# Kernel optimization log

Measured on AMD Instinct MI355X. Metric: run time of the kernel, lower is better.

Reference implementation:

```python
import jax, jax.numpy as jnp
import numpy as np
import math

B, S, D = 16, 256, 1024   # batch, seq (= s_model), d_model
HP, HC = 16, 8
DK, SK = D // HP, S // HC
EPS = 1e-6


def setup_inputs() -> dict:
    key = jax.random.key(0)
    ks = jax.random.split(key, 3)
    x = jax.random.normal(ks[0], (B, S, D), dtype=jnp.float32)
    Wp = jax.random.normal(ks[1], (3, D, D), dtype=jnp.float32) * 0.02  # (in,out)
    bp = jnp.zeros((3, D), dtype=jnp.float32)
    Wc = jax.random.normal(ks[2], (4, S, S), dtype=jnp.float32) * 0.02  # (in,out)
    bc = jnp.zeros((4, S), dtype=jnp.float32)
    a_p = jnp.ones((D,), dtype=jnp.float32)
    b_p = jnp.zeros((D,), dtype=jnp.float32)
    a_c = jnp.ones((S,), dtype=jnp.float32)
    b_c = jnp.zeros((S,), dtype=jnp.float32)
    return {"x": x, "Wp": Wp, "bp": bp, "Wc": Wc, "bc": bc,
            "a_p": a_p, "b_p": b_p, "a_c": a_c, "b_c": b_c}


def _std(x, axis):
    # torch .std(): unbiased (ddof=1)
    return jnp.std(x, axis=axis, keepdims=True, ddof=1)


def _attn(q, k, v):
    # q,k,v: [B, H, T, dk]; dropout is identity (eval)
    scores = jnp.einsum('bhtd,bhsd->bhts', q, k) / math.sqrt(q.shape[-1])
    p = jax.nn.softmax(scores, axis=-1)
    return jnp.einsum('bhts,bhsd->bhtd', p, v)


def reference(x, Wp, bp, Wc, bc, a_p, b_p, a_c, b_c):
    nb = x.shape[0]
    # ---- LayerNorm over channels (norm_p) ----
    mean = jnp.mean(x, axis=-1, keepdims=True)
    xp = a_p * (x - mean) / (_std(x, -1) + EPS) + b_p            # [B,S,D]
    # ---- positional attention over sequence ----
    qkv = jnp.einsum('bsd,nde->nbse', xp, Wp) + bp[:, None, None, :]
    q, k, v = [t.reshape(nb, S, HP, DK).transpose(0, 2, 1, 3) for t in qkv]
    xp = _attn(q, k, v).transpose(0, 2, 1, 3).reshape(nb, S, D)  # [B,S,D]
    # ---- LayerNorm_C: stats over sequence dim, affine indexed by seq ----
    mean_c = jnp.mean(xp, axis=-2, keepdims=True)                # [B,1,D]
    xc = a_c[:, None] * (xp - mean_c) / (_std(xp, -2) + EPS) + b_c[:, None]
    # ---- channel attention: channels are tokens, head dim SK ----
    xt = xc.transpose(0, 2, 1)                                    # [B,D,S]
    qkvc = jnp.einsum('bds,nse->nbde', xt, Wc[:3]) + bc[:3, None, None, :]
    qc, kc, vc = [t.reshape(nb, D, HC, SK).transpose(0, 2, 1, 3) for t in qkvc]
    xcatt = _attn(qc, kc, vc).transpose(0, 2, 1, 3).reshape(nb, D, S)  # [B,D,S]
    out = jnp.einsum('bds,se->bde', xcatt, Wc[3]) + bc[3]         # [B,D,S]
    return out.transpose(0, 2, 1)                                  # [B,S,D]
```

## Files before the change

### kernel.cpp

```cpp
#include <hip/hip_runtime.h>
#include <hip/hip_bf16.h>
#include <math.h>

#define B_ 16
#define S_ 256
#define D_ 1024
#define HP_ 16
#define DK_ 64
#define HC_ 8
#define SK_ 32
#define EPS_ 1e-6f

typedef __attribute__((ext_vector_type(8))) short short8v;
typedef __attribute__((ext_vector_type(4))) float f32x4;

__device__ __forceinline__ unsigned short f2bf(float f) {
    unsigned u = __float_as_uint(f);
    u += 0x7fffu + ((u >> 16) & 1u);
    return (unsigned short)(u >> 16);
}
__device__ __forceinline__ float bf2f(unsigned short h) {
    return __uint_as_float((unsigned)h << 16);
}
__device__ __forceinline__ ushort2 f2bf2(float a, float b) {
    __hip_bfloat162 h = __float22bfloat162_rn(make_float2(a, b));
    union { __hip_bfloat162 h2; ushort2 u2; } cv;
    cv.h2 = h;
    return cv.u2;
}
__device__ __forceinline__ void ldlds16(const unsigned short* g, unsigned short* l) {
    const unsigned int* gp = reinterpret_cast<const unsigned int*>(g);
    auto* lp = reinterpret_cast<__attribute__((address_space(3))) unsigned int*>(
        reinterpret_cast<uintptr_t>(l));
    __builtin_amdgcn_global_load_lds(gp, lp, 16, 0, 0);
}

__global__ __launch_bounds__(256) void k1_ln_p(
    const float* __restrict__ x, const float* __restrict__ a_p,
    const float* __restrict__ b_p, unsigned short* __restrict__ xh,
    unsigned short* __restrict__ xl)
{
    const int row = blockIdx.x;
    const float4* xr = (const float4*)(x + (size_t)row * D_);
    const int tid = threadIdx.x;
    float4 v = xr[tid];
    float s  = v.x + v.y + v.z + v.w;
    float sq = v.x*v.x + v.y*v.y + v.z*v.z + v.w*v.w;
    #pragma unroll
    for (int off = 32; off > 0; off >>= 1) {
        s  += __shfl_down(s, off);
        sq += __shfl_down(sq, off);
    }
    __shared__ float red[8];
    const int wid = tid >> 6, lane = tid & 63;
    if (lane == 0) { red[wid] = s; red[4 + wid] = sq; }
    __syncthreads();
    if (tid == 0) {
        float S0 = red[0] + red[1] + red[2] + red[3];
        float Q0 = red[4] + red[5] + red[6] + red[7];
        float mean = S0 / (float)D_;
        float var  = fmaxf((Q0 - (float)D_ * mean * mean) / (float)(D_ - 1), 0.0f);
        red[0] = mean;
        red[1] = 1.0f / (sqrtf(var) + EPS_);
    }
    __syncthreads();
    const float mean = red[0], inv = red[1];
    float4 a = ((const float4*)a_p)[tid];
    float4 b = ((const float4*)b_p)[tid];
    float o0 = a.x * (v.x - mean) * inv + b.x;
    float o1 = a.y * (v.y - mean) * inv + b.y;
    float o2 = a.z * (v.z - mean) * inv + b.z;
    float o3 = a.w * (v.w - mean) * inv + b.w;
    ushort2 h01 = f2bf2(o0, o1), h23 = f2bf2(o2, o3);
    ushort2 l01 = f2bf2(o0 - bf2f(h01.x), o1 - bf2f(h01.y));
    ushort2 l23 = f2bf2(o2 - bf2f(h23.x), o3 - bf2f(h23.y));
    ushort4 hv, lv;
    hv.x = h01.x; hv.y = h01.y; hv.z = h23.x; hv.w = h23.y;
    lv.x = l01.x; lv.y = l01.y; lv.z = l23.x; lv.w = l23.y;
    *(ushort4*)&xh[(size_t)row * D_ + tid*4] = hv;
    *(ushort4*)&xl[(size_t)row * D_ + tid*4] = lv;
}

__global__ __launch_bounds__(256) void tsplit(
    const float* __restrict__ W, unsigned short* __restrict__ Th,
    unsigned short* __restrict__ Tl, int K, int N)
{
    const int z = blockIdx.z;
    W  += (size_t)z * K * N;
    Th += (size_t)z * K * N;
    Tl += (size_t)z * K * N;
    const int k0 = blockIdx.x * 64, n0 = blockIdx.y * 64;
    __shared__ float tile[64][65];
    const int ix = threadIdx.x & 63, iy = threadIdx.x >> 6;
    #pragma unroll
    for (int u = 0; u < 16; u++) {
        const int kk = iy*16 + u;
        tile[kk][ix] = W[(size_t)(k0+kk)*N + n0 + ix];
    }
    __syncthreads();
    #pragma unroll
    for (int u = 0; u < 16; u += 2) {
        const int nn0 = iy*16 + u, nn1 = nn0 + 1;
        const float v0 = tile[ix][nn0], v1 = tile[ix][nn1];
        ushort2 h2 = f2bf2(v0, v1);
        ushort2 l2 = f2bf2(v0 - bf2f(h2.x), v1 - bf2f(h2.y));
        Th[(size_t)(n0+nn0)*K + k0 + ix] = h2.x;
        Th[(size_t)(n0+nn1)*K + k0 + ix] = h2.y;
        Tl[(size_t)(n0+nn0)*K + k0 + ix] = l2.x;
        Tl[(size_t)(n0+nn1)*K + k0 + ix] = l2.y;
    }
}

template<int OUTMODE>
__global__ __launch_bounds__(256) void mm_mfma(
    const unsigned short* __restrict__ Ah, const unsigned short* __restrict__ Al,
    const unsigned short* __restrict__ Bh, const unsigned short* __restrict__ Bl,
    const float* __restrict__ bias, void* __restrict__ Cout,
    int M, int N, int K, long sB, long sBias, long sC, long loff, int TB)
{
    const int z = blockIdx.z;
    Bh   += (size_t)z * sB;
    Bl   += (size_t)z * sB;
    bias += (size_t)z * sBias;
    const int n0 = blockIdx.x * 128, m0 = blockIdx.y * 128;
    __shared__ __align__(16) unsigned short Ash[128*32], Als[128*32];
    __shared__ __align__(16) unsigned short Bsh[128*32], Bls[128*32];
    const int tid = threadIdx.x;
    const int wave = tid >> 6, lane = tid & 63;
    const int wm = wave & 1, wn = wave >> 1;
    const int lrow = lane & 15, quad = lane >> 4;
    size_t gaOff[2], gbOff[2];
    int cb[2];
    #pragma unroll
    for (int j = 0; j < 2; j++) {
        const int p = wave*128 + j*64 + lane;
        const int row = p >> 2;
        const int cc = (p & 3) ^ ((row >> 1) & 3);
        gaOff[j] = (size_t)(m0 + row) * K + cc*8;
        gbOff[j] = (size_t)(n0 + row) * K + cc*8;
        cb[j] = (wave*128 + j*64) * 8;
    }
    int aFr[4], bFr[4];
    #pragma unroll
    for (int i = 0; i < 4; i++) {
        const int ra = wm*64 + i*16 + lrow;
        aFr[i] = ((ra << 2) | (quad ^ ((ra >> 1) & 3))) * 8;
        const int rb = wn*64 + i*16 + lrow;
        bFr[i] = ((rb << 2) | (quad ^ ((rb >> 1) & 3))) * 8;
    }
    f32x4 acc[4][4];
    #pragma unroll
    for (int j = 0; j < 4; j++) {
        const float bv = bias[n0 + wn*64 + j*16 + lrow];
        #pragma unroll
        for (int i = 0; i < 4; i++) {
            acc[i][j][0] = bv; acc[i][j][1] = bv; acc[i][j][2] = bv; acc[i][j][3] = bv;
        }
    }
    for (int k0 = 0; k0 < K; k0 += 32) {
        __syncthreads();
        #pragma unroll
        for (int j = 0; j < 2; j++) {
            ldlds16(Ah + gaOff[j] + k0, &Ash[cb[j]]);
            ldlds16(Al + gaOff[j] + k0, &Als[cb[j]]);
            ldlds16(Bh + gbOff[j] + k0, &Bsh[cb[j]]);
            ldlds16(Bl + gbOff[j] + k0, &Bls[cb[j]]);
        }
        __syncthreads();
        short8v bhf[4], blf[4];
        #pragma unroll
        for (int j = 0; j < 4; j++) {
            bhf[j] = *(const short8v*)&Bsh[bFr[j]];
            blf[j] = *(const short8v*)&Bls[bFr[j]];
        }
        #pragma unroll
        for (int i = 0; i < 4; i++) {
            short8v ahf = *(const short8v*)&Ash[aFr[i]];
            short8v alf = *(const short8v*)&Als[aFr[i]];
            #pragma unroll
            for (int j = 0; j < 4; j++) {
                acc[i][j] = __builtin_amdgcn_mfma_f32_16x16x32_bf16(ahf, bhf[j], acc[i][j], 0, 0, 0);
                acc[i][j] = __builtin_amdgcn_mfma_f32_16x16x32_bf16(ahf, blf[j], acc[i][j], 0, 0, 0);
                acc[i][j] = __builtin_amdgcn_mfma_f32_16x16x32_bf16(alf, bhf[j], acc[i][j], 0, 0, 0);
            }
        }
    }
    #pragma unroll
    for (int i = 0; i < 4; i++) {
        const int mrow = m0 + wm*64 + i*16 + quad*4;
        #pragma unroll
        for (int j = 0; j < 4; j++) {
            const int ncol = n0 + wn*64 + j*16 + lrow;
            if (OUTMODE == 0) {
                float* C = (float*)Cout + (size_t)z * sC;
                #pragma unroll
                for (int r = 0; r < 4; r++)
                    C[(size_t)(mrow + r) * N + ncol] = acc[i][j][r];
            } else if (OUTMODE == 1) {
                unsigned short* Ch = (unsigned short*)Cout + (size_t)z * sC;
                unsigned short* Cl = Ch + loff;
                #pragma unroll
                for (int r = 0; r < 4; r += 2) {
                    const float v0 = acc[i][j][r], v1 = acc[i][j][r+1];
                    ushort2 h2 = f2bf2(v0, v1);
                    ushort2 l2 = f2bf2(v0 - bf2f(h2.x), v1 - bf2f(h2.y));
                    Ch[(size_t)(mrow + r    ) * N + ncol] = h2.x;
                    Ch[(size_t)(mrow + r + 1) * N + ncol] = h2.y;
                    Cl[(size_t)(mrow + r    ) * N + ncol] = l2.x;
                    Cl[(size_t)(mrow + r + 1) * N + ncol] = l2.y;
                }
            } else if (OUTMODE == 2) {
                unsigned short* Ch = (unsigned short*)Cout;
                unsigned short* Cl = Ch + loff;
                const int bidx = mrow / TB, t0 = mrow % TB;
                const size_t ad = (size_t)bidx * N * TB + (size_t)ncol * TB + t0;
                const float v0 = acc[i][j][0], v1 = acc[i][j][1];
                const float v2 = acc[i][j][2], v3 = acc[i][j][3];
                ushort2 h01 = f2bf2(v0, v1), h23 = f2bf2(v2, v3);
                ushort2 l01 = f2bf2(v0 - bf2f(h01.x), v1 - bf2f(h01.y));
                ushort2 l23 = f2bf2(v2 - bf2f(h23.x), v3 - bf2f(h23.y));
                ushort4 hv, lv;
                hv.x = h01.x; hv.y = h01.y; hv.z = h23.x; hv.w = h23.y;
                lv.x = l01.x; lv.y = l01.y; lv.z = l23.x; lv.w = l23.y;
                *(ushort4*)&Ch[ad] = hv;
                *(ushort4*)&Cl[ad] = lv;
            } else {
                float* C = (float*)Cout;
                const int bidx = mrow / TB, t0 = mrow % TB;
                f32x4 a4 = acc[i][j];
                *(float4*)&C[((size_t)bidx * N + ncol) * TB + t0] = *(float4*)&a4;
            }
        }
    }
}

__global__ __launch_bounds__(256) void k3_mfma(
    const unsigned short* __restrict__ qh, const unsigned short* __restrict__ ql,
    const unsigned short* __restrict__ kh, const unsigned short* __restrict__ kl,
    const unsigned short* __restrict__ vth, const unsigned short* __restrict__ vtl,
    float* __restrict__ out)
{
    const int m0 = blockIdx.x * 64;
    const int h = blockIdx.y, b = blockIdx.z;
    const int hoff = h * DK_;
    const size_t rowb = (size_t)b * S_;
    __shared__ __align__(16) unsigned short Ksh[64*64], Ksl[64*64];
    __shared__ __align__(16) unsigned short VTh[64*64], VTl[64*64];
    __shared__ __align__(16) unsigned short Ps[64][72];
    const int tid = threadIdx.x;
    const int w = tid >> 6, lane = tid & 63;
    const int lrow = lane & 15, quad = lane >> 4;
    short8v bqh[2], bql[2];
    #pragma unroll
    for (int ks = 0; ks < 2; ks++) {
        const size_t qb = (rowb + m0 + w*16 + lrow) * D_ + hoff + ks*32 + quad*8;
        bqh[ks] = *(const short8v*)&qh[qb];
        bql[ks] = *(const short8v*)&ql[qb];
    }
    size_t kOff[2], vOff[2];
    int cb[2];
    #pragma unroll
    for (int j = 0; j < 2; j++) {
        const int p = w*128 + j*64 + lane;
        const int row = p >> 3;
        const int cc = (p & 7) ^ (row & 7);
        kOff[j] = (rowb + row) * D_ + hoff + cc*8;
        vOff[j] = ((size_t)b * D_ + hoff + row) * S_ + cc*8;
        cb[j] = (w*128 + j*64) * 8;
    }
    f32x4 o[4] = {};
    float lacc = 0.f;
    for (int kt = 0; kt < 4; kt++) {
        const int n00 = kt * 64;
        __syncthreads();
        #pragma unroll
        for (int j = 0; j < 2; j++) {
            ldlds16(kh  + kOff[j] + (size_t)n00 * D_, &Ksh[cb[j]]);
            ldlds16(kl  + kOff[j] + (size_t)n00 * D_, &Ksl[cb[j]]);
            ldlds16(vth + vOff[j] + n00,              &VTh[cb[j]]);
            ldlds16(vtl + vOff[j] + n00,              &VTl[cb[j]]);
        }
        __syncthreads();
        f32x4 sa[4] = {};
        #pragma unroll
        for (int ks = 0; ks < 2; ks++) {
            #pragma unroll
            for (int jk = 0; jk < 4; jk++) {
                const int r = jk*16 + lrow, c = ks*4 + quad;
                const int off = ((r << 3) | (c ^ (r & 7))) * 8;
                short8v akh = *(const short8v*)&Ksh[off];
                short8v akl = *(const short8v*)&Ksl[off];
                sa[jk] = __builtin_amdgcn_mfma_f32_16x16x32_bf16(akh, bqh[ks], sa[jk], 0, 0, 0);
                sa[jk] = __builtin_amdgcn_mfma_f32_16x16x32_bf16(akl, bqh[ks], sa[jk], 0, 0, 0);
                sa[jk] = __builtin_amdgcn_mfma_f32_16x16x32_bf16(akh, bql[ks], sa[jk], 0, 0, 0);
            }
        }
        #pragma unroll
        for (int jk = 0; jk < 4; jk++) {
            float p0 = __expf(sa[jk][0] * 0.125f);
            float p1 = __expf(sa[jk][1] * 0.125f);
            float p2 = __expf(sa[jk][2] * 0.125f);
            float p3 = __expf(sa[jk][3] * 0.125f);
            lacc += (p0 + p1) + (p2 + p3);
            ushort2 p01 = f2bf2(p0, p1), p23 = f2bf2(p2, p3);
            ushort4 ph;
            ph.x = p01.x; ph.y = p01.y; ph.z = p23.x; ph.w = p23.y;
            *(ushort4*)&Ps[w*16 + lrow][jk*16 + quad*4] = ph;
        }
        #pragma unroll
        for (int ks = 0; ks < 2; ks++) {
            short8v ap = *(const short8v*)&Ps[w*16 + lrow][ks*32 + quad*8];
            #pragma unroll
            for (int nf = 0; nf < 4; nf++) {
                const int r = nf*16 + lrow, c = ks*4 + quad;
                const int off = ((r << 3) | (c ^ (r & 7))) * 8;
                short8v vH = *(const short8v*)&VTh[off];
                short8v vL = *(const short8v*)&VTl[off];
                o[nf] = __builtin_amdgcn_mfma_f32_16x16x32_bf16(ap, vH, o[nf], 0, 0, 0);
                o[nf] = __builtin_amdgcn_mfma_f32_16x16x32_bf16(ap, vL, o[nf], 0, 0, 0);
            }
        }
    }
    lacc += __shfl_xor(lacc, 16);
    lacc += __shfl_xor(lacc, 32);
    #pragma unroll
    for (int r = 0; r < 4; r++) {
        const float linv = 1.0f / __shfl(lacc, quad*4 + r);
        #pragma unroll
        for (int nf = 0; nf < 4; nf++)
            out[(rowb + m0 + w*16 + quad*4 + r) * D_ + hoff + nf*16 + lrow] =
                o[nf][r] * linv;
    }
}

__global__ __launch_bounds__(256) void k6_mfma(
    const unsigned short* __restrict__ qch, const unsigned short* __restrict__ qcl,
    const unsigned short* __restrict__ kch, const unsigned short* __restrict__ kcl,
    const unsigned short* __restrict__ vth, const unsigned short* __restrict__ vtl,
    unsigned short* __restrict__ oh, unsigned short* __restrict__ ol)
{
    const int m0 = blockIdx.x * 128;
    const int h = blockIdx.y, b = blockIdx.z;
    const int hoff = h * SK_;
    const size_t rowb = (size_t)b * D_;
    __shared__ __align__(16) unsigned short Ksh[64*32], Ksl[64*32];
    __shared__ __align__(16) unsigned short VTh[32*64], VTl[32*64];
    __shared__ __align__(16) unsigned short Ps[128][72];
    const int tid = threadIdx.x;
    const int w = tid >> 6, lane = tid & 63;
    const int lrow = lane & 15, quad = lane >> 4;
    short8v bqh[2], bql[2];
    #pragma unroll
    for (int i = 0; i < 2; i++) {
        const size_t qb = (rowb + m0 + w*32 + i*16 + lrow) * S_ + hoff + quad*8;
        bqh[i] = *(const short8v*)&qch[qb];
        bql[i] = *(const short8v*)&qcl[qb];
    }
    size_t kOff, vOff;
    {
        const int pK = w*64 + lane;
        const int rowK = pK >> 2;
        const int ccK = (pK & 3) ^ ((rowK >> 1) & 3);
        kOff = (rowb + rowK) * S_ + hoff + ccK*8;
        const int pV = w*64 + lane;
        const int rowV = pV >> 3;
        const int ccV = (pV & 7) ^ (rowV & 7);
        vOff = ((size_t)b * S_ + hoff + rowV) * D_ + ccV*8;
    }
    const int cb = w*64*8;
    f32x4 o[2][2] = {};
    float lacc[2] = {0.f, 0.f};
    for (int kt = 0; kt < 16; kt++) {
        const int n00 = kt * 64;
        __syncthreads();
        ldlds16(kch + kOff + (size_t)n00 * S_, &Ksh[cb]);
        ldlds16(kcl + kOff + (size_t)n00 * S_, &Ksl[cb]);
        ldlds16(vth + vOff + n00,              &VTh[cb]);
        ldlds16(vtl + vOff + n00,              &VTl[cb]);
        __syncthreads();
        f32x4 sa[2][4] = {};
        #pragma unroll
        for (int jk = 0; jk < 4; jk++) {
            const int r = jk*16 + lrow;
            const int off = ((r << 2) | (quad ^ ((r >> 1) & 3))) * 8;
            short8v akh = *(const short8v*)&Ksh[off];
            short8v akl = *(const short8v*)&Ksl[off];
            #pragma unroll
            for (int i = 0; i < 2; i++) {
                sa[i][jk] = __builtin_amdgcn_mfma_f32_16x16x32_bf16(akh, bqh[i], sa[i][jk], 0, 0, 0);
                sa[i][jk] = __builtin_amdgcn_mfma_f32_16x16x32_bf16(akl, bqh[i], sa[i][jk], 0, 0, 0);
                sa[i][jk] = __builtin_amdgcn_mfma_f32_16x16x32_bf16(akh, bql[i], sa[i][jk], 0, 0, 0);
            }
        }
        #pragma unroll
        for (int i = 0; i < 2; i++)
            #pragma unroll
            for (int jk = 0; jk < 4; jk++) {
                float p0 = __expf(sa[i][jk][0] * 0.17677669529663687f);
                float p1 = __expf(sa[i][jk][1] * 0.17677669529663687f);
                float p2 = __expf(sa[i][jk][2] * 0.17677669529663687f);
                float p3 = __expf(sa[i][jk][3] * 0.17677669529663687f);
                lacc[i] += (p0 + p1) + (p2 + p3);
                ushort2 p01 = f2bf2(p0, p1), p23 = f2bf2(p2, p3);
                ushort4 ph;
                ph.x = p01.x; ph.y = p01.y; ph.z = p23.x; ph.w = p23.y;
                *(ushort4*)&Ps[w*32 + i*16 + lrow][jk*16 + quad*4] = ph;
            }
        #pragma unroll
        for (int ks = 0; ks < 2; ks++) {
            short8v ap[2];
            #pragma unroll
            for (int i = 0; i < 2; i++)
                ap[i] = *(const short8v*)&Ps[w*32 + i*16 + lrow][ks*32 + quad*8];
            #pragma unroll
            for (int nf = 0; nf < 2; nf++) {
                const int r = nf*16 + lrow, c = ks*4 + quad;
                const int off = ((r << 3) | (c ^ (r & 7))) * 8;
                short8v vHf = *(const short8v*)&VTh[off];
                short8v vLf = *(const short8v*)&VTl[off];
                #pragma unroll
                for (int i = 0; i < 2; i++) {
                    o[i][nf] = __builtin_amdgcn_mfma_f32_16x16x32_bf16(ap[i], vHf, o[i][nf], 0, 0, 0);
                    o[i][nf] = __builtin_amdgcn_mfma_f32_16x16x32_bf16(ap[i], vLf, o[i][nf], 0, 0, 0);
                }
            }
        }
    }
    #pragma unroll
    for (int i = 0; i < 2; i++) {
        lacc[i] += __shfl_xor(lacc[i], 16);
        lacc[i] += __shfl_xor(lacc[i], 32);
    }
    #pragma unroll
    for (int i = 0; i < 2; i++)
        #pragma unroll
        for (int r = 0; r < 4; r++) {
            const float linv = 1.0f / __shfl(lacc[i], quad*4 + r);
            const float v0 = o[i][0][r] * linv;
            const float v1 = o[i][1][r] * linv;
            ushort2 h2 = f2bf2(v0, v1);
            ushort2 l2 = f2bf2(v0 - bf2f(h2.x), v1 - bf2f(h2.y));
            const size_t idx =
                (rowb + m0 + w*32 + i*16 + quad*4 + r) * S_ + hoff + lrow;
            oh[idx]      = h2.x;
            oh[idx + 16] = h2.y;
            ol[idx]      = l2.x;
            ol[idx + 16] = l2.y;
        }
}

__global__ __launch_bounds__(256) void k4_fused(
    const float* __restrict__ x, const float* __restrict__ a_c,
    const float* __restrict__ b_c, unsigned short* __restrict__ xth,
    unsigned short* __restrict__ xtl)
{
    const int d0 = blockIdx.x * 64, b = blockIdx.y;
    __shared__ float tile[256][65];
    __shared__ float part[8][64];
    __shared__ float stats[2][64];
    __shared__ float acs[256], bcs[256];
    const int tid = threadIdx.x;
    acs[tid] = a_c[tid];
    bcs[tid] = b_c[tid];
    const int dl = tid & 63, sq = tid >> 6;
    float s1 = 0.f, s2 = 0.f;
    #pragma unroll 8
    for (int u = 0; u < 64; u++) {
        const int srow = sq*64 + u;
        const float v = x[((size_t)(b*S_ + srow))*D_ + d0 + dl];
        tile[srow][dl] = v;
        s1 += v; s2 += v*v;
    }
    part[sq][dl] = s1; part[4+sq][dl] = s2;
    __syncthreads();
    if (tid < 64) {
        const float S = part[0][tid]+part[1][tid]+part[2][tid]+part[3][tid];
        const float Q = part[4][tid]+part[5][tid]+part[6][tid]+part[7][tid];
        const float mean = S / (float)S_;
        const float var  = fmaxf((Q - (float)S_*mean*mean)/(float)(S_-1), 0.f);
        stats[0][tid] = mean;
        stats[1][tid] = 1.f/(sqrtf(var)+EPS_);
    }
    __syncthreads();
    const int dd = tid >> 2, s00 = (tid & 3) * 64;
    const float mean = stats[0][dd], inv = stats[1][dd];
    const size_t obase = ((size_t)(b*D_ + d0 + dd))*S_ + s00;
    #pragma unroll
    for (int c = 0; c < 8; c++) {
        union { ushort u[8]; uint4 v4; } hb, lb;
        #pragma unroll
        for (int t = 0; t < 8; t += 2) {
            const int s = s00 + c*8 + t;
            const float v0 = acs[s]  *(tile[s][dd]  -mean)*inv + bcs[s];
            const float v1 = acs[s+1]*(tile[s+1][dd]-mean)*inv + bcs[s+1];
            ushort2 h2 = f2bf2(v0, v1);
            ushort2 l2 = f2bf2(v0 - bf2f(h2.x), v1 - bf2f(h2.y));
            hb.u[t] = h2.x; hb.u[t+1] = h2.y;
            lb.u[t] = l2.x; lb.u[t+1] = l2.y;
        }
        *(uint4*)&xth[obase + c*8] = hb.v4;
        *(uint4*)&xtl[obase + c*8] = lb.v4;
    }
}

extern "C" void kernel_launch(void* const* d_in, const int* in_sizes, int n_in,
                              void* d_out, int out_size, void* d_ws, size_t ws_size,
                              hipStream_t stream)
{
    const float* x   = (const float*)d_in[0];
    const float* Wp  = (const float*)d_in[1];
    const float* bp  = (const float*)d_in[2];
    const float* Wc  = (const float*)d_in[3];
    const float* bc  = (const float*)d_in[4];
    const float* a_p = (const float*)d_in[5];
    const float* b_p = (const float*)d_in[6];
    const float* a_c = (const float*)d_in[7];
    const float* b_c = (const float*)d_in[8];
    float* out = (float*)d_out;
    float* ws  = (float*)d_ws;
    const size_t NE = (size_t)B_ * S_ * D_;

    float* S0 = ws;
    float* S1 = ws + NE;
    float* S2 = ws + 2*NE;
    float* S3 = ws + 3*NE;
    unsigned short* SW = (unsigned short*)(ws + 4*NE);

    const size_t baseBytes = 4*NE*sizeof(float);
    const bool big = ws_size >= baseBytes + (size_t)2 * 3 * D_ * D_ * sizeof(unsigned short) * 2;

    unsigned short* xh = (unsigned short*)S0;
    unsigned short* xl = xh + NE;
    unsigned short* q_h  = (unsigned short*)S1;
    unsigned short* k_h  = (unsigned short*)S2;
    unsigned short* vt_h = (unsigned short*)S3;

    k1_ln_p<<<dim3(B_*S_), 256, 0, stream>>>(x, a_p, b_p, xh, xl);

    if (big) {
        unsigned short* WTh = SW;
        unsigned short* WTl = WTh + (size_t)3 * D_ * D_;
        tsplit<<<dim3(D_/64, D_/64, 3), 256, 0, stream>>>(Wp, WTh, WTl, D_, D_);
        mm_mfma<1><<<dim3(D_/128, (B_*S_)/128, 2), 256, 0, stream>>>(
            xh, xl, WTh, WTl, bp, (void*)q_h,
            B_*S_, D_, D_, (long)D_*D_, (long)D_, (long)(2*NE), (long)NE, 1);
        mm_mfma<2><<<dim3(D_/128, (B_*S_)/128, 1), 256, 0, stream>>>(
            xh, xl, WTh + (size_t)2*D_*D_, WTl + (size_t)2*D_*D_, bp + 2*D_,
            (void*)vt_h, B_*S_, D_, D_, 0, 0, 0, (long)NE, S_);
    } else {
        unsigned short* WTh = SW;
        unsigned short* WTl = WTh + (size_t)D_ * D_;
        for (int z = 0; z < 3; z++) {
            tsplit<<<dim3(D_/64, D_/64, 1), 256, 0, stream>>>(
                Wp + (size_t)z*D_*D_, WTh, WTl, D_, D_);
            if (z < 2)
                mm_mfma<1><<<dim3(D_/128, (B_*S_)/128, 1), 256, 0, stream>>>(
                    xh, xl, WTh, WTl, bp + (size_t)z*D_,
                    (void*)(q_h + (size_t)z*2*NE),
                    B_*S_, D_, D_, 0, 0, 0, (long)NE, 1);
            else
                mm_mfma<2><<<dim3(D_/128, (B_*S_)/128, 1), 256, 0, stream>>>(
                    xh, xl, WTh, WTl, bp + (size_t)z*D_, (void*)vt_h,
                    B_*S_, D_, D_, 0, 0, 0, (long)NE, S_);
        }
    }

    k3_mfma<<<dim3(S_/64, HP_, B_), 256, 0, stream>>>(
        q_h, q_h + NE, k_h, k_h + NE, vt_h, vt_h + NE, S0);

    unsigned short* xth = (unsigned short*)S1;
    k4_fused<<<dim3(D_/64, B_), 256, 0, stream>>>(S0, a_c, b_c, xth, xth + NE);

    unsigned short* WcTh = SW;
    unsigned short* WcTl = WcTh + (size_t)4 * S_ * S_;
    tsplit<<<dim3(S_/64, S_/64, 4), 256, 0, stream>>>(Wc, WcTh, WcTl, S_, S_);
    unsigned short* qc_h  = (unsigned short*)S2;
    unsigned short* vct_h = (unsigned short*)S0;
    mm_mfma<1><<<dim3(S_/128, (B_*D_)/128, 2), 256, 0, stream>>>(
        xth, xth + NE, WcTh, WcTl, bc, (void*)qc_h,
        B_*D_, S_, S_, (long)S_*S_, (long)S_, (long)(2*NE), (long)NE, 1);
    mm_mfma<2><<<dim3(S_/128, (B_*D_)/128, 1), 256, 0, stream>>>(
        xth, xth + NE, WcTh + (size_t)2*S_*S_, WcTl + (size_t)2*S_*S_, bc + 2*S_,
        (void*)vct_h, B_*D_, S_, S_, 0, 0, 0, (long)NE, D_);

    unsigned short* kc_h = (unsigned short*)S3;
    unsigned short* xch  = (unsigned short*)S1;
    k6_mfma<<<dim3(D_/128, HC_, B_), 256, 0, stream>>>(
        qc_h, qc_h + NE, kc_h, kc_h + NE, vct_h, vct_h + NE, xch, xch + NE);

    mm_mfma<3><<<dim3(S_/128, (B_*D_)/128, 1), 256, 0, stream>>>(
        xch, xch + NE, WcTh + (size_t)3*S_*S_, WcTl + (size_t)3*S_*S_, bc + 3*S_,
        (void*)out, B_*D_, S_, S_, 0, 0, 0, 0, D_);
}
```

Baseline: 356.5 us.

## Double-buffer attention K/V tiles, fold softmax scale into QK projections, swizzle blocks

Both attention kernels now use two LDS buffers for K/V, so the next tile's global-to-LDS load is issued before computing on the current one. The two full barriers per iteration become a single waitcnt plus barrier. The softmax scale times log2(e) is split as a square root into the Q and K projection epilogues, which lets the kernels call a raw v_exp_f32 instead of __expf with a multiply. The block index mapping is also remapped so that consecutive workgroups are spread across batch/head. The costs are doubled LDS use, which may reduce occupancy, and slightly different rounding of Q and K.

```diff
diff --git a/kernel.cpp b/kernel.cpp
--- a/kernel.cpp
+++ b/kernel.cpp
@@ -11,6 +11,9 @@
 #define SK_ 32
 #define EPS_ 1e-6f
 
+#define ALPHA_P 0.42466089973135876f
+#define ALPHA_C 0.50500991942f
+
 typedef __attribute__((ext_vector_type(8))) short short8v;
 typedef __attribute__((ext_vector_type(4))) float f32x4;
 
@@ -27,6 +30,11 @@
     union { __hip_bfloat162 h2; ushort2 u2; } cv;
     cv.h2 = h;
     return cv.u2;
+}
+__device__ __forceinline__ float exp2_fast(float x) {
+    float r;
+    asm("v_exp_f32 %0, %1\n\ts_nop 0" : "=v"(r) : "v"(x));
+    return r;
 }
 __device__ __forceinline__ void ldlds16(const unsigned short* g, unsigned short* l) {
     const unsigned int* gp = reinterpret_cast<const unsigned int*>(g);
@@ -116,7 +124,8 @@
     const unsigned short* __restrict__ Ah, const unsigned short* __restrict__ Al,
     const unsigned short* __restrict__ Bh, const unsigned short* __restrict__ Bl,
     const float* __restrict__ bias, void* __restrict__ Cout,
-    int M, int N, int K, long sB, long sBias, long sC, long loff, int TB)
+    int M, int N, int K, long sB, long sBias, long sC, long loff, int TB,
+    float alpha)
 {
     const int z = blockIdx.z;
     Bh   += (size_t)z * sB;
@@ -201,7 +210,8 @@
                 unsigned short* Cl = Ch + loff;
                 #pragma unroll
                 for (int r = 0; r < 4; r += 2) {
-                    const float v0 = acc[i][j][r], v1 = acc[i][j][r+1];
+                    const float v0 = acc[i][j][r] * alpha;
+                    const float v1 = acc[i][j][r+1] * alpha;
                     ushort2 h2 = f2bf2(v0, v1);
                     ushort2 l2 = f2bf2(v0 - bf2f(h2.x), v1 - bf2f(h2.y));
                     Ch[(size_t)(mrow + r    ) * N + ncol] = h2.x;
@@ -240,12 +250,15 @@
     const unsigned short* __restrict__ vth, const unsigned short* __restrict__ vtl,
     float* __restrict__ out)
 {
-    const int m0 = blockIdx.x * 64;
-    const int h = blockIdx.y, b = blockIdx.z;
+    const int flat = blockIdx.x + (blockIdx.y << 2) + (blockIdx.z << 6);
+    const int logical = ((flat & 7) << 7) | (flat >> 3);
+    const int m0 = (logical & 3) * 64;
+    const int h  = (logical >> 2) & 15;
+    const int b  = logical >> 6;
     const int hoff = h * DK_;
     const size_t rowb = (size_t)b * S_;
-    __shared__ __align__(16) unsigned short Ksh[64*64], Ksl[64*64];
-    __shared__ __align__(16) unsigned short VTh[64*64], VTl[64*64];
+    __shared__ __align__(16) unsigned short Ksh[2][64*64], Ksl[2][64*64];
+    __shared__ __align__(16) unsigned short VTh[2][64*64], VTl[2][64*64];
     __shared__ __align__(16) unsigned short Ps[64][72];
     const int tid = threadIdx.x;
     const int w = tid >> 6, lane = tid & 63;
@@ -270,17 +283,27 @@
     }
     f32x4 o[4] = {};
     float lacc = 0.f;
+    #pragma unroll
+    for (int j = 0; j < 2; j++) {
+        ldlds16(kh  + kOff[j], &Ksh[0][cb[j]]);
+        ldlds16(kl  + kOff[j], &Ksl[0][cb[j]]);
+        ldlds16(vth + vOff[j], &VTh[0][cb[j]]);
+        ldlds16(vtl + vOff[j], &VTl[0][cb[j]]);
+    }
     for (int kt = 0; kt < 4; kt++) {
-        const int n00 = kt * 64;
-        __syncthreads();
-        #pragma unroll
-        for (int j = 0; j < 2; j++) {
-            ldlds16(kh  + kOff[j] + (size_t)n00 * D_, &Ksh[cb[j]]);
-            ldlds16(kl  + kOff[j] + (size_t)n00 * D_, &Ksl[cb[j]]);
-            ldlds16(vth + vOff[j] + n00,              &VTh[cb[j]]);
-            ldlds16(vtl + vOff[j] + n00,              &VTl[cb[j]]);
-        }
-        __syncthreads();
+        const int cur = kt & 1;
+        asm volatile("s_waitcnt vmcnt(0)" ::: "memory");
+        asm volatile("s_barrier" ::: "memory");
+        if (kt < 3) {
+            const int n01 = (kt + 1) * 64;
+            #pragma unroll
+            for (int j = 0; j < 2; j++) {
+                ldlds16(kh  + kOff[j] + (size_t)n01 * D_, &Ksh[cur^1][cb[j]]);
+                ldlds16(kl  + kOff[j] + (size_t)n01 * D_, &Ksl[cur^1][cb[j]]);
+                ldlds16(vth + vOff[j] + n01,              &VTh[cur^1][cb[j]]);
+                ldlds16(vtl + vOff[j] + n01,              &VTl[cur^1][cb[j]]);
+            }
+        }
         f32x4 sa[4] = {};
         #pragma unroll
         for (int ks = 0; ks < 2; ks++) {
@@ -288,8 +311,8 @@
             for (int jk = 0; jk < 4; jk++) {
                 const int r = jk*16 + lrow, c = ks*4 + quad;
                 const int off = ((r << 3) | (c ^ (r & 7))) * 8;
-                short8v akh = *(const short8v*)&Ksh[off];
-                short8v akl = *(const short8v*)&Ksl[off];
+                short8v akh = *(const short8v*)&Ksh[cur][off];
+                short8v akl = *(const short8v*)&Ksl[cur][off];
                 sa[jk] = __builtin_amdgcn_mfma_f32_16x16x32_bf16(akh, bqh[ks], sa[jk], 0, 0, 0);
                 sa[jk] = __builtin_amdgcn_mfma_f32_16x16x32_bf16(akl, bqh[ks], sa[jk], 0, 0, 0);
                 sa[jk] = __builtin_amdgcn_mfma_f32_16x16x32_bf16(akh, bql[ks], sa[jk], 0, 0, 0);
@@ -297,10 +320,10 @@
         }
         #pragma unroll
         for (int jk = 0; jk < 4; jk++) {
-            float p0 = __expf(sa[jk][0] * 0.125f);
-            float p1 = __expf(sa[jk][1] * 0.125f);
-            float p2 = __expf(sa[jk][2] * 0.125f);
-            float p3 = __expf(sa[jk][3] * 0.125f);
+            float p0 = exp2_fast(sa[jk][0]);
+            float p1 = exp2_fast(sa[jk][1]);
+            float p2 = exp2_fast(sa[jk][2]);
+            float p3 = exp2_fast(sa[jk][3]);
             lacc += (p0 + p1) + (p2 + p3);
             ushort2 p01 = f2bf2(p0, p1), p23 = f2bf2(p2, p3);
             ushort4 ph;
@@ -314,8 +337,8 @@
             for (int nf = 0; nf < 4; nf++) {
                 const int r = nf*16 + lrow, c = ks*4 + quad;
                 const int off = ((r << 3) | (c ^ (r & 7))) * 8;
-                short8v vH = *(const short8v*)&VTh[off];
-                short8v vL = *(const short8v*)&VTl[off];
+                short8v vH = *(const short8v*)&VTh[cur][off];
+                short8v vL = *(const short8v*)&VTl[cur][off];
                 o[nf] = __builtin_amdgcn_mfma_f32_16x16x32_bf16(ap, vH, o[nf], 0, 0, 0);
                 o[nf] = __builtin_amdgcn_mfma_f32_16x16x32_bf16(ap, vL, o[nf], 0, 0, 0);
             }
@@ -339,12 +362,15 @@
     const unsigned short* __restrict__ vth, const unsigned short* __restrict__ vtl,
     unsigned short* __restrict__ oh, unsigned short* __restrict__ ol)
 {
-    const int m0 = blockIdx.x * 128;
-    const int h = blockIdx.y, b = blockIdx.z;
+    const int flat = blockIdx.x + (blockIdx.y << 3) + (blockIdx.z << 6);
+    const int logical = ((flat & 7) << 7) | (flat >> 3);
+    const int m0 = (logical & 7) << 7;
+    const int h  = (logical >> 3) & 7;
+    const int b  = logical >> 6;
     const int hoff = h * SK_;
     const size_t rowb = (size_t)b * D_;
-    __shared__ __align__(16) unsigned short Ksh[64*32], Ksl[64*32];
-    __shared__ __align__(16) unsigned short VTh[32*64], VTl[32*64];
+    __shared__ __align__(16) unsigned short Ksh[2][64*32], Ksl[2][64*32];
+    __shared__ __align__(16) unsigned short VTh[2][32*64], VTl[2][32*64];
     __shared__ __align__(16) unsigned short Ps[128][72];
     const int tid = threadIdx.x;
     const int w = tid >> 6, lane = tid & 63;
@@ -370,21 +396,28 @@
     const int cb = w*64*8;
     f32x4 o[2][2] = {};
     float lacc[2] = {0.f, 0.f};
+    ldlds16(kch + kOff, &Ksh[0][cb]);
+    ldlds16(kcl + kOff, &Ksl[0][cb]);
+    ldlds16(vth + vOff, &VTh[0][cb]);
+    ldlds16(vtl + vOff, &VTl[0][cb]);
     for (int kt = 0; kt < 16; kt++) {
-        const int n00 = kt * 64;
-        __syncthreads();
-        ldlds16(kch + kOff + (size_t)n00 * S_, &Ksh[cb]);
-        ldlds16(kcl + kOff + (size_t)n00 * S_, &Ksl[cb]);
-        ldlds16(vth + vOff + n00,              &VTh[cb]);
-        ldlds16(vtl + vOff + n00,              &VTl[cb]);
-        __syncthreads();
+        const int cur = kt & 1;
+        asm volatile("s_waitcnt vmcnt(0)" ::: "memory");
+        asm volatile("s_barrier" ::: "memory");
+        if (kt < 15) {
+            const int n01 = (kt + 1) * 64;
+            ldlds16(kch + kOff + (size_t)n01 * S_, &Ksh[cur^1][cb]);
+            ldlds16(kcl + kOff + (size_t)n01 * S_, &Ksl[cur^1][cb]);
+            ldlds16(vth + vOff + n01,              &VTh[cur^1][cb]);
+            ldlds16(vtl + vOff + n01,              &VTl[cur^1][cb]);
+        }
         f32x4 sa[2][4] = {};
         #pragma unroll
         for (int jk = 0; jk < 4; jk++) {
             const int r = jk*16 + lrow;
             const int off = ((r << 2) | (quad ^ ((r >> 1) & 3))) * 8;
-            short8v akh = *(const short8v*)&Ksh[off];
-            short8v akl = *(const short8v*)&Ksl[off];
+            short8v akh = *(const short8v*)&Ksh[cur][off];
+            short8v akl = *(const short8v*)&Ksl[cur][off];
             #pragma unroll
             for (int i = 0; i < 2; i++) {
                 sa[i][jk] = __builtin_amdgcn_mfma_f32_16x16x32_bf16(akh, bqh[i], sa[i][jk], 0, 0, 0);
@@ -396,10 +429,10 @@
         for (int i = 0; i < 2; i++)
             #pragma unroll
             for (int jk = 0; jk < 4; jk++) {
-                float p0 = __expf(sa[i][jk][0] * 0.17677669529663687f);
-                float p1 = __expf(sa[i][jk][1] * 0.17677669529663687f);
-                float p2 = __expf(sa[i][jk][2] * 0.17677669529663687f);
-                float p3 = __expf(sa[i][jk][3] * 0.17677669529663687f);
+                float p0 = exp2_fast(sa[i][jk][0]);
+                float p1 = exp2_fast(sa[i][jk][1]);
+                float p2 = exp2_fast(sa[i][jk][2]);
+                float p3 = exp2_fast(sa[i][jk][3]);
                 lacc[i] += (p0 + p1) + (p2 + p3);
                 ushort2 p01 = f2bf2(p0, p1), p23 = f2bf2(p2, p3);
                 ushort4 ph;
@@ -416,8 +449,8 @@
             for (int nf = 0; nf < 2; nf++) {
                 const int r = nf*16 + lrow, c = ks*4 + quad;
                 const int off = ((r << 3) | (c ^ (r & 7))) * 8;
-                short8v vHf = *(const short8v*)&VTh[off];
-                short8v vLf = *(const short8v*)&VTl[off];
+                short8v vHf = *(const short8v*)&VTh[cur][off];
+                short8v vLf = *(const short8v*)&VTl[cur][off];
                 #pragma unroll
                 for (int i = 0; i < 2; i++) {
                     o[i][nf] = __builtin_amdgcn_mfma_f32_16x16x32_bf16(ap[i], vHf, o[i][nf], 0, 0, 0);
@@ -543,10 +576,10 @@
         tsplit<<<dim3(D_/64, D_/64, 3), 256, 0, stream>>>(Wp, WTh, WTl, D_, D_);
         mm_mfma<1><<<dim3(D_/128, (B_*S_)/128, 2), 256, 0, stream>>>(
             xh, xl, WTh, WTl, bp, (void*)q_h,
-            B_*S_, D_, D_, (long)D_*D_, (long)D_, (long)(2*NE), (long)NE, 1);
+            B_*S_, D_, D_, (long)D_*D_, (long)D_, (long)(2*NE), (long)NE, 1, ALPHA_P);
         mm_mfma<2><<<dim3(D_/128, (B_*S_)/128, 1), 256, 0, stream>>>(
             xh, xl, WTh + (size_t)2*D_*D_, WTl + (size_t)2*D_*D_, bp + 2*D_,
-            (void*)vt_h, B_*S_, D_, D_, 0, 0, 0, (long)NE, S_);
+            (void*)vt_h, B_*S_, D_, D_, 0, 0, 0, (long)NE, S_, 1.0f);
     } else {
         unsigned short* WTh = SW;
         unsigned short* WTl = WTh + (size_t)D_ * D_;
@@ -557,11 +590,11 @@
                 mm_mfma<1><<<dim3(D_/128, (B_*S_)/128, 1), 256, 0, stream>>>(
                     xh, xl, WTh, WTl, bp + (size_t)z*D_,
                     (void*)(q_h + (size_t)z*2*NE),
-                    B_*S_, D_, D_, 0, 0, 0, (long)NE, 1);
+                    B_*S_, D_, D_, 0, 0, 0, (long)NE, 1, ALPHA_P);
             else
                 mm_mfma<2><<<dim3(D_/128, (B_*S_)/128, 1), 256, 0, stream>>>(
                     xh, xl, WTh, WTl, bp + (size_t)z*D_, (void*)vt_h,
-                    B_*S_, D_, D_, 0, 0, 0, (long)NE, S_);
+                    B_*S_, D_, D_, 0, 0, 0, (long)NE, S_, 1.0f);
         }
     }
 
@@ -578,10 +611,10 @@
     unsigned short* vct_h = (unsigned short*)S0;
     mm_mfma<1><<<dim3(S_/128, (B_*D_)/128, 2), 256, 0, stream>>>(
         xth, xth + NE, WcTh, WcTl, bc, (void*)qc_h,
-        B_*D_, S_, S_, (long)S_*S_, (long)S_, (long)(2*NE), (long)NE, 1);
+        B_*D_, S_, S_, (long)S_*S_, (long)S_, (long)(2*NE), (long)NE, 1, ALPHA_C);
     mm_mfma<2><<<dim3(S_/128, (B_*D_)/128, 1), 256, 0, stream>>>(
         xth, xth + NE, WcTh + (size_t)2*S_*S_, WcTl + (size_t)2*S_*S_, bc + 2*S_,
-        (void*)vct_h, B_*D_, S_, S_, 0, 0, 0, (long)NE, D_);
+        (void*)vct_h, B_*D_, S_, S_, 0, 0, 0, (long)NE, D_, 1.0f);
 
     unsigned short* kc_h = (unsigned short*)S3;
     unsigned short* xch  = (unsigned short*)S1;
@@ -590,5 +623,5 @@
 
     mm_mfma<3><<<dim3(S_/128, (B_*D_)/128, 1), 256, 0, stream>>>(
         xch, xch + NE, WcTh + (size_t)3*S_*S_, WcTl + (size_t)3*S_*S_, bc + 3*S_,
-        (void*)out, B_*D_, S_, S_, 0, 0, 0, 0, D_);
-}
+        (void*)out, B_*D_, S_, S_, 0, 0, 0, 0, D_, 1.0f);
+}
```

New measurement: 338.2 us. 1.05x faster.
